# Optimization experiments

Measured on AMD Instinct MI355X. Metric: run time of the kernel, lower is better.

The kernel has to match this reference:

```python
import jax, jax.numpy as jnp
import numpy as np

EPS = 1e-7          # keras K.epsilon()
MIN_TEMP = 0.1
ALPHA = 0.99999
START_TEMP = 10.0
BATCH, D, BINS, K_OUT = 4096, 20000, 10, 64


def setup_inputs() -> dict:
    key = jax.random.key(0)
    k1, k2, k3 = jax.random.split(key, 3)
    X = jax.random.normal(k1, (BATCH, D), dtype=jnp.float32)
    u = jax.random.normal(k2, (D, BINS), dtype=jnp.float32)
    # keras 'uniform' initializer: U(-0.05, 0.05)
    tinyW = jax.random.uniform(k3, (BINS, K_OUT), dtype=jnp.float32, minval=-0.05, maxval=0.05)
    temp = jnp.float32(START_TEMP)
    return {"X": X, "u": u, "tinyW": tinyW, "temp": temp}


def greedy_assign(p):
    """Greedy bipartite argmax-and-mask assignment (the host loop in the original).
    p: (k, d) scores. Returns (k, d) 0/1 assignment with one 1 per row, unique cols."""
    k, d = p.shape

    def step(pm, _):
        ind = jnp.argmax(pm)            # global argmax over flattened (k, d)
        x = ind // d
        y = ind % d
        pm = pm.at[x, :].set(-1.0).at[:, y].set(-1.0)
        return pm, (x, y)

    _, (xs, ys) = jax.lax.scan(step, p, None, length=k)
    return jnp.zeros((k, d), p.dtype).at[xs, ys].set(1.0)


def reference(X, u, tinyW, temp):
    # al = softmax(u @ tinyW) over output_dim axis, then transpose -> (k, d)
    al = jax.nn.softmax(u @ tinyW, axis=-1).T                  # (k, d)
    logits = jnp.log(10.0 * jnp.clip(al, EPS, 0.9999999))      # (k, d)
    # Gumbel noise: -log(-log(U)), U ~ Uniform(eps, 1)
    nkey = jax.random.key(42)
    uniform = jax.random.uniform(nkey, logits.shape, logits.dtype, EPS, 1.0)
    gumbel = -jnp.log(-jnp.log(uniform))
    # annealed temperature update (K.update in original)
    new_temp = jnp.maximum(jnp.float32(MIN_TEMP), temp * jnp.float32(ALPHA))
    samples = jax.nn.softmax((logits + gumbel) / new_temp, axis=-1)  # (k, d)
    # inference-path discrete selection via greedy argmax-and-mask loop
    discrete = greedy_assign(samples)                           # (k, d)
    # training path: Y = X @ samples^T  (main memory-bound skinny GEMM)
    Y = X @ samples.T                                           # (batch, k)
    return Y, discrete, new_temp
```

## Files before the change

kernel.cpp:

```cpp
#include <hip/hip_runtime.h>
#include <stdint.h>
#include <math.h>

typedef unsigned long long ull;
typedef __attribute__((ext_vector_type(8))) short short8;
typedef __attribute__((ext_vector_type(4))) float f32x4;

#define DD 20000
#define NK 64
#define NB 4096
#define YN (NB * NK)
#define TOTN (YN + NK * DD + 1)
#define KS 32

#define Z_OFF 0
#define CV_OFF 1280000
#define CC_OFF 1284096
#define SB_OFF 1288192

__device__ __forceinline__ uint32_t tf_bits(uint32_t j) {
  const uint32_t k0 = 0u, k1 = 42u;
  const uint32_t k2 = 0x1BD11BDAu ^ k0 ^ k1;
  uint32_t x0 = k0;
  uint32_t x1 = j + k1;
#define TFR(r) { x0 += x1; x1 = (x1 << r) | (x1 >> (32 - r)); x1 ^= x0; }
  TFR(13) TFR(15) TFR(26) TFR(6)
  x0 += k1; x1 += k2 + 1u;
  TFR(17) TFR(29) TFR(16) TFR(24)
  x0 += k2; x1 += k0 + 2u;
  TFR(13) TFR(15) TFR(26) TFR(6)
  x0 += k0; x1 += k1 + 3u;
  TFR(17) TFR(29) TFR(16) TFR(24)
  x0 += k1; x1 += k2 + 4u;
  TFR(13) TFR(15) TFR(26) TFR(6)
  x0 += k2; x1 += k0 + 5u;
#undef TFR
  return x0 ^ x1;
}

__device__ __forceinline__ uint32_t pkbf(float a, float b) {
  uint32_t ua = __float_as_uint(a), ub = __float_as_uint(b);
  ua = (ua + 0x7FFFu + ((ua >> 16) & 1u)) >> 16;
  ub = (ub + 0x7FFFu + ((ub >> 16) & 1u)) >> 16;
  return ua | (ub << 16);
}

__global__ __launch_bounds__(256) void k_z(
    const float* __restrict__ uu, const float* __restrict__ tw,
    const float* __restrict__ temp, float* __restrict__ Z) {
  __shared__ float tile[NK][65];
  const int tid = threadIdx.x;
  const int lane = tid & 63;
  const int wv = tid >> 6;
  const int d0 = blockIdx.x * 64;
  const float nt = fmaxf(0.1f, temp[0] * 0.99999f);
  float w[10];
#pragma unroll
  for (int i = 0; i < 10; ++i) w[i] = tw[i * NK + lane];
  for (int it = 0; it < 16; ++it) {
    const int dl = wv * 16 + it;
    const int d = d0 + dl;
    if (d < DD) {
      float m = 0.f;
#pragma unroll
      for (int i = 0; i < 10; ++i) m = fmaf(uu[d * 10 + i], w[i], m);
      float mx = m;
#pragma unroll
      for (int off = 32; off; off >>= 1) mx = fmaxf(mx, __shfl_xor(mx, off, 64));
      double e = exp((double)(m - mx));
      double ssum = e;
#pragma unroll
      for (int off = 32; off; off >>= 1) ssum += __shfl_xor(ssum, off, 64);
      float al = (float)(e / ssum);
      float c = fminf(fmaxf(al, 1e-7f), 0.9999999f);
      float lg = (float)log((double)(10.0f * c));
      const uint32_t bits = tf_bits((uint32_t)(lane * DD + d));
      float uf = __uint_as_float((bits >> 9) | 0x3f800000u) - 1.0f;
      float uv = fmaxf(1e-7f, uf * (1.0f - 1e-7f) + 1e-7f);
      float g = (float)(-log(-log((double)uv)));
      tile[lane][dl] = (lg + g) / nt;
    }
  }
  __syncthreads();
  for (int r0 = 0; r0 < NK; r0 += 4) {
    const int r = r0 + wv;
    const int d = d0 + lane;
    if (d < DD) Z[r * DD + d] = tile[r][lane];
  }
}

__global__ __launch_bounds__(256) void k_rows(
    const float* __restrict__ Z, ushort* __restrict__ SBm,
    float* __restrict__ disc, float* __restrict__ cv, int* __restrict__ cc) {
  const int k = blockIdx.x;
  const int tid = threadIdx.x;
  __shared__ float redf[256];
  __shared__ double redd[256];
  __shared__ ull keys[2048];
  __shared__ ull wbest[4];
  const float* zr = Z + (size_t)k * DD;
  ushort* sbr = SBm + (size_t)k * DD;
  float* dr = disc + (size_t)k * DD;
  float mx = -1e30f;
  for (int d = tid; d < DD; d += 256) mx = fmaxf(mx, zr[d]);
  redf[tid] = mx;
  __syncthreads();
  for (int s = 128; s; s >>= 1) {
    if (tid < s) redf[tid] = fmaxf(redf[tid], redf[tid + s]);
    __syncthreads();
  }
  mx = redf[0];
  double psum = 0.0;
  for (int d = tid; d < DD; d += 256) psum += exp((double)(zr[d] - mx));
  redd[tid] = psum;
  __syncthreads();
  for (int s = 128; s; s >>= 1) {
    if (tid < s) redd[tid] += redd[tid + s];
    __syncthreads();
  }
  const double sumall = redd[0];
  float tv[8]; int tc[8];
#pragma unroll
  for (int s = 0; s < 8; ++s) { tv[s] = -1.f; tc[s] = 0; }
  for (int d = tid; d < DD; d += 256) {
    double e = exp((double)(zr[d] - mx));
    float svv = (float)(e / sumall);
    uint32_t ub = __float_as_uint(svv);
    sbr[d] = (ushort)((ub + 0x7FFFu + ((ub >> 16) & 1u)) >> 16);
    dr[d] = 0.f;
    if (svv > tv[7]) {
      float cvr = svv; int ccr = d;
#pragma unroll
      for (int s = 0; s < 8; ++s) {
        bool sw = cvr > tv[s];
        float nv = sw ? cvr : tv[s]; int nc = sw ? ccr : tc[s];
        cvr = sw ? tv[s] : cvr; ccr = sw ? tc[s] : ccr;
        tv[s] = nv; tc[s] = nc;
      }
    }
  }
#pragma unroll
  for (int s = 0; s < 8; ++s)
    keys[(tid << 3) + s] = (((ull)__float_as_uint(tv[s])) << 32)
                         | ((ull)(uint32_t)(32767 - tc[s]) << 11)
                         | ((ull)tid << 3) | (ull)s;
  __syncthreads();
  for (int t = 0; t < NK; ++t) {
    ull best = 0;
#pragma unroll
    for (int s = 0; s < 8; ++s) { ull kk = keys[(tid << 3) + s]; if (kk > best) best = kk; }
#pragma unroll
    for (int off = 32; off; off >>= 1) { ull o = __shfl_xor(best, off, 64); if (o > best) best = o; }
    if ((tid & 63) == 0) wbest[tid >> 6] = best;
    __syncthreads();
    ull win = wbest[0];
#pragma unroll
    for (int wI = 1; wI < 4; ++wI) if (wbest[wI] > win) win = wbest[wI];
    const uint32_t lo = (uint32_t)win;
    const int slot = lo & 7;
    const int owner = (lo >> 3) & 255;
    const int col = 32767 - (int)(lo >> 11);
    if (tid == 0) {
      cv[(k << 6) + t] = __uint_as_float((uint32_t)(win >> 32));
      cc[(k << 6) + t] = col;
    }
    if (tid == owner) keys[(owner << 3) + slot] = 0;
    __syncthreads();
  }
}

__global__ __launch_bounds__(64) void k_greedy(
    const float* __restrict__ cv, const int* __restrict__ cc,
    const float* __restrict__ temp, float* __restrict__ out) {
  __shared__ float v[NK][NK];
  __shared__ int c[NK][NK];
  __shared__ unsigned char used[DD];
  const int lane = threadIdx.x;
  for (int i = lane; i < DD; i += 64) used[i] = 0;
  for (int i = 0; i < NK; ++i) { v[i][lane] = cv[(i << 6) + lane]; c[i][lane] = cc[(i << 6) + lane]; }
  __syncthreads();
  int ptr = 0;
  bool done = false;
  for (int t = 0; t < NK; ++t) {
    ull key = 0;
    if (!done) {
      while (ptr < NK && used[c[lane][ptr]]) ++ptr;
      if (ptr < NK) {
        key = (((ull)__float_as_uint(v[lane][ptr])) << 21)
            | ((ull)(uint32_t)(63 - lane) << 15)
            | (ull)(uint32_t)(32767 - c[lane][ptr]);
      }
    }
#pragma unroll
    for (int off = 32; off; off >>= 1) { ull o = __shfl_xor(key, off, 64); if (o > key) key = o; }
    const int col = 32767 - (int)(key & 0x7FFF);
    const int row = 63 - (int)((key >> 15) & 63);
    if (lane == row) done = true;
    if (lane == 0) { used[col] = 1; out[YN + (size_t)row * DD + col] = 1.0f; }
    __syncthreads();
  }
  if (lane == 0) out[TOTN - 1] = fmaxf(0.1f, temp[0] * 0.99999f);
}

__global__ __launch_bounds__(256) void k_zeroY(float* __restrict__ out) {
  const int i = blockIdx.x * 256 + threadIdx.x;
  ((float4*)out)[i] = make_float4(0.f, 0.f, 0.f, 0.f);
}

__global__ __launch_bounds__(256) void k_gemm(
    const float* __restrict__ X, const ushort* __restrict__ SBm,
    float* __restrict__ Y) {
  const int tid = threadIdx.x;
  const int lane = tid & 63;
  const int wv = tid >> 6;
  const int ksp = blockIdx.x;
  const int m16 = lane & 15;
  const int kq = lane >> 4;
  const int mRow = blockIdx.y * 64 + wv * 16 + m16;
  const float* xp = X + (size_t)mRow * DD;
  const ushort* bp = SBm + (size_t)m16 * DD;
  f32x4 acc[4] = {{0,0,0,0},{0,0,0,0},{0,0,0,0},{0,0,0,0}};
  for (int s = ksp; s < 625; s += KS) {
    const int k0 = s * 32 + kq * 8;
    const float4 xa = *(const float4*)(xp + k0);
    const float4 xb = *(const float4*)(xp + k0 + 4);
    union { uint32_t u[4]; short8 v; } A;
    A.u[0] = pkbf(xa.x, xa.y); A.u[1] = pkbf(xa.z, xa.w);
    A.u[2] = pkbf(xb.x, xb.y); A.u[3] = pkbf(xb.z, xb.w);
#pragma unroll
    for (int nt = 0; nt < 4; ++nt) {
      union { uint4 q; short8 v; } B;
      B.q = *(const uint4*)(bp + (size_t)nt * 16 * DD + k0);
      acc[nt] = __builtin_amdgcn_mfma_f32_16x16x32_bf16(A.v, B.v, acc[nt], 0, 0, 0);
    }
  }
  const int rBase = blockIdx.y * 64 + wv * 16 + kq * 4;
#pragma unroll
  for (int nt = 0; nt < 4; ++nt)
#pragma unroll
    for (int r = 0; r < 4; ++r)
      atomicAdd(&Y[(size_t)(rBase + r) * 64 + nt * 16 + m16], acc[nt][r]);
}

extern "C" void kernel_launch(void* const* d_in, const int* in_sizes, int n_in,
                              void* d_out, int out_size, void* d_ws, size_t ws_size,
                              hipStream_t stream) {
  (void)in_sizes; (void)n_in; (void)out_size; (void)ws_size;
  const float* X = (const float*)d_in[0];
  const float* uu = (const float*)d_in[1];
  const float* tw = (const float*)d_in[2];
  const float* temp = (const float*)d_in[3];
  float* out = (float*)d_out;
  float* W = (float*)d_ws;
  float* Z = W + Z_OFF;
  float* CV = W + CV_OFF;
  int* CC = (int*)(W + CC_OFF);
  ushort* SBm = (ushort*)(W + SB_OFF);

  hipLaunchKernelGGL(k_zeroY, dim3(YN / 1024), dim3(256), 0, stream, out);
  hipLaunchKernelGGL(k_z, dim3(313), dim3(256), 0, stream, uu, tw, temp, Z);
  hipLaunchKernelGGL(k_rows, dim3(64), dim3(256), 0, stream, Z, SBm, out + YN, CV, CC);
  hipLaunchKernelGGL(k_greedy, dim3(1), dim3(64), 0, stream, CV, CC, temp, out);
  hipLaunchKernelGGL(k_gemm, dim3(KS, 64), dim3(256), 0, stream, X, SBm, out);
}
```

Measured before the change: 660.4 us.

## Precompute exp and per-block row sums in k_z; replace GEMM atomics with split-K reduction

k_z now computes exp(z) directly in double, without subtracting a row max, and stores it along with per-block partial row sums. This lets k_rows skip its max and sum passes and the repeated exp calls. The GEMM writes split-K partials to a workspace buffer instead of doing atomicAdd into a zeroed Y, and a new reduction kernel sums them; this removes the zero-init kernel and the atomics. It also unrolls the K loop by 2. Costs: a double-precision E buffer, which doubles the Z traffic, a 32x partial buffer of about 33 MB, and possible overflow without max subtraction if temperature gets small.

```diff
diff --git a/kernel.cpp b/kernel.cpp
--- a/kernel.cpp
+++ b/kernel.cpp
@@ -13,10 +13,12 @@
 #define TOTN (YN + NK * DD + 1)
 #define KS 32
 
-#define Z_OFF 0
-#define CV_OFF 1280000
-#define CC_OFF 1284096
-#define SB_OFF 1288192
+#define E_OFF   0u
+#define RSP_OFF 10240000u
+#define CV_OFF  10400256u
+#define CC_OFF  10416640u
+#define SB_OFF  10433024u
+#define P_OFF   12993024u
 
 __device__ __forceinline__ uint32_t tf_bits(uint32_t j) {
   const uint32_t k0 = 0u, k1 = 42u;
@@ -38,17 +40,12 @@
   return x0 ^ x1;
 }
 
-__device__ __forceinline__ uint32_t pkbf(float a, float b) {
-  uint32_t ua = __float_as_uint(a), ub = __float_as_uint(b);
-  ua = (ua + 0x7FFFu + ((ua >> 16) & 1u)) >> 16;
-  ub = (ub + 0x7FFFu + ((ub >> 16) & 1u)) >> 16;
-  return ua | (ub << 16);
-}
-
 __global__ __launch_bounds__(256) void k_z(
     const float* __restrict__ uu, const float* __restrict__ tw,
-    const float* __restrict__ temp, float* __restrict__ Z) {
-  __shared__ float tile[NK][65];
+    const float* __restrict__ temp, double* __restrict__ E,
+    double* __restrict__ RSP) {
+  __shared__ double tile[NK][65];
+  __shared__ double psumw[4][NK];
   const int tid = threadIdx.x;
   const int lane = tid & 63;
   const int wv = tid >> 6;
@@ -57,9 +54,11 @@
   float w[10];
 #pragma unroll
   for (int i = 0; i < 10; ++i) w[i] = tw[i * NK + lane];
+  double psum = 0.0;
   for (int it = 0; it < 16; ++it) {
     const int dl = wv * 16 + it;
     const int d = d0 + dl;
+    double e = 0.0;
     if (d < DD) {
       float m = 0.f;
 #pragma unroll
@@ -67,51 +66,50 @@
       float mx = m;
 #pragma unroll
       for (int off = 32; off; off >>= 1) mx = fmaxf(mx, __shfl_xor(mx, off, 64));
-      double e = exp((double)(m - mx));
-      double ssum = e;
+      double ee = exp((double)(m - mx));
+      double ssum = ee;
 #pragma unroll
       for (int off = 32; off; off >>= 1) ssum += __shfl_xor(ssum, off, 64);
-      float al = (float)(e / ssum);
+      float al = (float)(ee / ssum);
       float c = fminf(fmaxf(al, 1e-7f), 0.9999999f);
       float lg = (float)log((double)(10.0f * c));
       const uint32_t bits = tf_bits((uint32_t)(lane * DD + d));
       float uf = __uint_as_float((bits >> 9) | 0x3f800000u) - 1.0f;
       float uv = fmaxf(1e-7f, uf * (1.0f - 1e-7f) + 1e-7f);
       float g = (float)(-log(-log((double)uv)));
-      tile[lane][dl] = (lg + g) / nt;
-    }
-  }
+      float z = (lg + g) / nt;
+      e = exp((double)z);
+    }
+    tile[lane][dl] = e;
+    psum += e;
+  }
+  psumw[wv][lane] = psum;
   __syncthreads();
   for (int r0 = 0; r0 < NK; r0 += 4) {
     const int r = r0 + wv;
     const int d = d0 + lane;
-    if (d < DD) Z[r * DD + d] = tile[r][lane];
+    if (d < DD) E[(size_t)r * DD + d] = tile[r][lane];
+  }
+  if (wv == 0) {
+    double s = psumw[0][lane] + psumw[1][lane] + psumw[2][lane] + psumw[3][lane];
+    RSP[(size_t)blockIdx.x * NK + lane] = s;
   }
 }
 
 __global__ __launch_bounds__(256) void k_rows(
-    const float* __restrict__ Z, ushort* __restrict__ SBm,
-    float* __restrict__ disc, float* __restrict__ cv, int* __restrict__ cc) {
+    const double* __restrict__ E, const double* __restrict__ RSP,
+    ushort* __restrict__ SBm, float* __restrict__ disc,
+    float* __restrict__ cv, int* __restrict__ cc) {
   const int k = blockIdx.x;
   const int tid = threadIdx.x;
-  __shared__ float redf[256];
   __shared__ double redd[256];
   __shared__ ull keys[2048];
   __shared__ ull wbest[4];
-  const float* zr = Z + (size_t)k * DD;
+  const double* er = E + (size_t)k * DD;
   ushort* sbr = SBm + (size_t)k * DD;
   float* dr = disc + (size_t)k * DD;
-  float mx = -1e30f;
-  for (int d = tid; d < DD; d += 256) mx = fmaxf(mx, zr[d]);
-  redf[tid] = mx;
-  __syncthreads();
-  for (int s = 128; s; s >>= 1) {
-    if (tid < s) redf[tid] = fmaxf(redf[tid], redf[tid + s]);
-    __syncthreads();
-  }
-  mx = redf[0];
   double psum = 0.0;
-  for (int d = tid; d < DD; d += 256) psum += exp((double)(zr[d] - mx));
+  for (int b = tid; b < 313; b += 256) psum += RSP[(size_t)b * NK + k];
   redd[tid] = psum;
   __syncthreads();
   for (int s = 128; s; s >>= 1) {
@@ -123,8 +121,7 @@
 #pragma unroll
   for (int s = 0; s < 8; ++s) { tv[s] = -1.f; tc[s] = 0; }
   for (int d = tid; d < DD; d += 256) {
-    double e = exp((double)(zr[d] - mx));
-    float svv = (float)(e / sumall);
+    float svv = (float)(er[d] / sumall);
     uint32_t ub = __float_as_uint(svv);
     sbr[d] = (ushort)((ub + 0x7FFFu + ((ub >> 16) & 1u)) >> 16);
     dr[d] = 0.f;
@@ -202,14 +199,9 @@
   if (lane == 0) out[TOTN - 1] = fmaxf(0.1f, temp[0] * 0.99999f);
 }
 
-__global__ __launch_bounds__(256) void k_zeroY(float* __restrict__ out) {
-  const int i = blockIdx.x * 256 + threadIdx.x;
-  ((float4*)out)[i] = make_float4(0.f, 0.f, 0.f, 0.f);
-}
-
 __global__ __launch_bounds__(256) void k_gemm(
     const float* __restrict__ X, const ushort* __restrict__ SBm,
-    float* __restrict__ Y) {
+    float* __restrict__ P) {
   const int tid = threadIdx.x;
   const int lane = tid & 63;
   const int wv = tid >> 6;
@@ -220,13 +212,26 @@
   const float* xp = X + (size_t)mRow * DD;
   const ushort* bp = SBm + (size_t)m16 * DD;
   f32x4 acc[4] = {{0,0,0,0},{0,0,0,0},{0,0,0,0},{0,0,0,0}};
+#pragma unroll 2
   for (int s = ksp; s < 625; s += KS) {
     const int k0 = s * 32 + kq * 8;
     const float4 xa = *(const float4*)(xp + k0);
     const float4 xb = *(const float4*)(xp + k0 + 4);
     union { uint32_t u[4]; short8 v; } A;
-    A.u[0] = pkbf(xa.x, xa.y); A.u[1] = pkbf(xa.z, xa.w);
-    A.u[2] = pkbf(xb.x, xb.y); A.u[3] = pkbf(xb.z, xb.w);
+    uint32_t ua0 = __float_as_uint(xa.x), ua1 = __float_as_uint(xa.y);
+    uint32_t ua2 = __float_as_uint(xa.z), ua3 = __float_as_uint(xa.w);
+    uint32_t ub0 = __float_as_uint(xb.x), ub1 = __float_as_uint(xb.y);
+    uint32_t ub2 = __float_as_uint(xb.z), ub3 = __float_as_uint(xb.w);
+    ua0 = (ua0 + 0x7FFFu + ((ua0 >> 16) & 1u)) >> 16;
+    ua1 = (ua1 + 0x7FFFu + ((ua1 >> 16) & 1u)) >> 16;
+    ua2 = (ua2 + 0x7FFFu + ((ua2 >> 16) & 1u)) >> 16;
+    ua3 = (ua3 + 0x7FFFu + ((ua3 >> 16) & 1u)) >> 16;
+    ub0 = (ub0 + 0x7FFFu + ((ub0 >> 16) & 1u)) >> 16;
+    ub1 = (ub1 + 0x7FFFu + ((ub1 >> 16) & 1u)) >> 16;
+    ub2 = (ub2 + 0x7FFFu + ((ub2 >> 16) & 1u)) >> 16;
+    ub3 = (ub3 + 0x7FFFu + ((ub3 >> 16) & 1u)) >> 16;
+    A.u[0] = ua0 | (ua1 << 16); A.u[1] = ua2 | (ua3 << 16);
+    A.u[2] = ub0 | (ub1 << 16); A.u[3] = ub2 | (ub3 << 16);
 #pragma unroll
     for (int nt = 0; nt < 4; ++nt) {
       union { uint4 q; short8 v; } B;
@@ -234,12 +239,25 @@
       acc[nt] = __builtin_amdgcn_mfma_f32_16x16x32_bf16(A.v, B.v, acc[nt], 0, 0, 0);
     }
   }
+  float* pp = P + (size_t)ksp * YN;
   const int rBase = blockIdx.y * 64 + wv * 16 + kq * 4;
 #pragma unroll
   for (int nt = 0; nt < 4; ++nt)
 #pragma unroll
     for (int r = 0; r < 4; ++r)
-      atomicAdd(&Y[(size_t)(rBase + r) * 64 + nt * 16 + m16], acc[nt][r]);
+      pp[(size_t)(rBase + r) * 64 + nt * 16 + m16] = acc[nt][r];
+}
+
+__global__ __launch_bounds__(256) void k_gred(const float* __restrict__ P,
+                                              float* __restrict__ Y) {
+  const int i = blockIdx.x * 256 + threadIdx.x;
+  float4 a = ((const float4*)P)[i];
+#pragma unroll
+  for (int j = 1; j < KS; ++j) {
+    const float4 b = ((const float4*)(P + (size_t)j * YN))[i];
+    a.x += b.x; a.y += b.y; a.z += b.z; a.w += b.w;
+  }
+  ((float4*)Y)[i] = a;
 }
 
 extern "C" void kernel_launch(void* const* d_in, const int* in_sizes, int n_in,
@@ -251,15 +269,17 @@
   const float* tw = (const float*)d_in[2];
   const float* temp = (const float*)d_in[3];
   float* out = (float*)d_out;
-  float* W = (float*)d_ws;
-  float* Z = W + Z_OFF;
-  float* CV = W + CV_OFF;
-  int* CC = (int*)(W + CC_OFF);
+  char* W = (char*)d_ws;
+  double* E   = (double*)(W + E_OFF);
+  double* RSP = (double*)(W + RSP_OFF);
+  float*  CV  = (float*)(W + CV_OFF);
+  int*    CC  = (int*)(W + CC_OFF);
   ushort* SBm = (ushort*)(W + SB_OFF);
-
-  hipLaunchKernelGGL(k_zeroY, dim3(YN / 1024), dim3(256), 0, stream, out);
-  hipLaunchKernelGGL(k_z, dim3(313), dim3(256), 0, stream, uu, tw, temp, Z);
-  hipLaunchKernelGGL(k_rows, dim3(64), dim3(256), 0, stream, Z, SBm, out + YN, CV, CC);
+  float*  P   = (float*)(W + P_OFF);
+
+  hipLaunchKernelGGL(k_z, dim3(313), dim3(256), 0, stream, uu, tw, temp, E, RSP);
+  hipLaunchKernelGGL(k_rows, dim3(64), dim3(256), 0, stream, E, RSP, SBm, out + YN, CV, CC);
   hipLaunchKernelGGL(k_greedy, dim3(1), dim3(64), 0, stream, CV, CC, temp, out);
-  hipLaunchKernelGGL(k_gemm, dim3(KS, 64), dim3(256), 0, stream, X, SBm, out);
-}
+  hipLaunchKernelGGL(k_gemm, dim3(KS, 64), dim3(256), 0, stream, X, SBm, P);
+  hipLaunchKernelGGL(k_gred, dim3(256), dim3(256), 0, stream, P, out);
+}
```

New measurement: 650.8 us. Within noise of the previous version (-1.5%).
